# Kernel optimization log

Measured on AMD Instinct MI355X. Metric: run time of the kernel, lower is better.

The kernel has to match this reference:

```python
import jax, jax.numpy as jnp
import numpy as np

NEG_INF = -jnp.inf


def setup_inputs() -> dict:
    key = jax.random.key(0)
    ks = jax.random.split(key, 20)
    B, N, M = 8, 1024, 128
    F_OP, F_MA, F_E, OUT, HID = 64, 64, 16, 64, 128
    inp = {
        "x": jax.random.normal(ks[0], (B, N, F_OP), dtype=jnp.float32),
        "y": jax.random.normal(ks[1], (B, M, F_MA), dtype=jnp.float32),
        "z": jax.random.normal(ks[2], (B, N, M, F_E), dtype=jnp.float32),
        "op_adj_in": jax.random.randint(ks[3], (B, N, N), 0, 2, dtype=jnp.int32),
        "ma_adj_in": jax.random.randint(ks[4], (B, N, N), 0, 2, dtype=jnp.int32),
        "op_ma_adj": jax.random.randint(ks[5], (B, N, M), 0, 2, dtype=jnp.int32),
        # learned parameters
        "weight_op": jax.random.normal(ks[6], (F_OP, OUT), dtype=jnp.float32) * 0.1,
        "weight_ma": jax.random.normal(ks[7], (F_MA, OUT), dtype=jnp.float32) * 0.1,
        "weight_edge": jax.random.normal(ks[8], (F_E, OUT), dtype=jnp.float32) * 0.1,
        "attention_op": jax.random.normal(ks[9], (1, 2 * OUT), dtype=jnp.float32) * 0.1,
        "attention_ma": jax.random.normal(ks[10], (1, 3 * OUT), dtype=jnp.float32) * 0.1,
        "w1": jax.random.normal(ks[11], (2 * OUT, HID), dtype=jnp.float32) * 0.1,
        "b1": jnp.zeros((HID,), dtype=jnp.float32),
        "w2": jax.random.normal(ks[12], (HID, HID), dtype=jnp.float32) * 0.1,
        "b2": jnp.zeros((HID,), dtype=jnp.float32),
        "wo": jax.random.normal(ks[13], (HID, OUT), dtype=jnp.float32) * 0.1,
        "bo": jnp.zeros((OUT,), dtype=jnp.float32),
    }
    return inp


def reference(x, y, z, op_adj_in, ma_adj_in, op_ma_adj,
              weight_op, weight_ma, weight_edge, attention_op, attention_ma,
              w1, b1, w2, b2, wo, bo):
    OUT = weight_op.shape[1]
    h = jnp.einsum('bni,io->bno', x, weight_op)  # [B,N,OUT]
    # all_combinations[b,i,j] = cat(h[b,j], h[b,i]); dot with attention_op splits:
    a1 = attention_op[0, :OUT]
    a2 = attention_op[0, OUT:]
    e_op = (h @ a2)[:, :, None] + (h @ a1)[:, None, :]  # [B,N,N]
    e_op = jax.nn.leaky_relu(e_op, negative_slope=0.01)

    adj = (jnp.swapaxes(op_adj_in, 1, 2) + op_adj_in
           + jnp.swapaxes(ma_adj_in, 1, 2) + ma_adj_in)  # [B,N,N]
    row_mask = jnp.all(op_ma_adj == 0, axis=-1)  # [B,N] ops with no machine link
    adj = jnp.where(row_mask[:, :, None], 1, adj)
    att = jnp.where(adj > 0, e_op, NEG_INF)
    attention_in_op = jax.nn.softmax(att, axis=2)
    h_prime_op = jnp.einsum('bij,bjo->bio', attention_in_op, h)  # [B,N,OUT]

    h_ma = jnp.einsum('bmi,io->bmo', y, weight_ma)  # [B,M,OUT]
    h_edge = jnp.einsum('bnmi,io->bnmo', z, weight_edge)  # [B,N,M,OUT]
    # cat([h_op_i, h_ma_j, h_edge_ij]) @ attention_ma split into three dots
    am1 = attention_ma[0, :OUT]
    am2 = attention_ma[0, OUT:2 * OUT]
    am3 = attention_ma[0, 2 * OUT:]
    e_ma = (h @ am1)[:, :, None] + (h_ma @ am2)[:, None, :] + h_edge @ am3  # [B,N,M]
    e_ma = jax.nn.leaky_relu(e_ma, negative_slope=0.01)

    adj2 = jnp.where(row_mask[:, :, None], 1, op_ma_adj)
    att2 = jnp.where(adj2 > 0, e_ma, NEG_INF)
    attention_in_ma = jax.nn.softmax(att2, axis=2)  # [B,N,M]
    h_ma_edge = h_ma[:, None, :, :] + h_edge  # [B,N,M,OUT]
    h_prime_ma = jnp.einsum('bnm,bnmo->bno', attention_in_ma, h_ma_edge) + h

    h_prime = jnp.concatenate([h_prime_op, h_prime_ma], axis=-1)  # [B,N,2*OUT]
    embed = jax.nn.elu(h_prime @ w1 + b1)
    embed = jax.nn.elu(embed @ w2 + b2)
    embed = embed @ wo + bo
    embed = jnp.where(row_mask[:, :, None], 0.0, embed)
    return embed
```

## Files before the change

### kernel.cpp

```cpp
#include <hip/hip_runtime.h>
#include <math.h>

#define BB 8
#define NN 1024
#define MM 128
#define FOUT 64
#define HIDN 128

#define OFF_H       0
#define OFF_HMA     524288
#define OFF_HA1     589824
#define OFF_HA2     598016
#define OFF_HAM1    606208
#define OFF_HMAAM2  614400
#define OFF_RMASK   615424
#define OFF_WAM3    623616
#define OFF_HPRIME  623632
#define OFF_RDIR    1672208
#define OFF_OPMB    1934352
#define OFF_WT1HI   1967120
#define OFF_WT1LO   1975312
#define OFF_WT2HI   1983504
#define OFF_WT2LO   1991696
#define OFF_WTOHI   1999888
#define OFF_WTOLO   2003984
#define OFF_HTHI    2008080
#define OFF_HTLO    2270224
#define OFF_HMATHI  2532368
#define OFF_HMATLO  2565136
#define OFF_TRM     2597904

typedef __attribute__((ext_vector_type(8))) short bf16x8;
typedef __attribute__((ext_vector_type(8))) unsigned short u16x8;
typedef __attribute__((ext_vector_type(4))) float f32x4;

__device__ __forceinline__ void splitbf(float v, unsigned short& h, unsigned short& l) {
    unsigned u = __float_as_uint(v);
    unsigned hb = (u + 0x7FFFu + ((u >> 16) & 1u)) >> 16;
    float hf = __uint_as_float(hb << 16);
    float lf = v - hf;
    unsigned ul = __float_as_uint(lf);
    unsigned lb = (ul + 0x7FFFu + ((ul >> 16) & 1u)) >> 16;
    h = (unsigned short)hb; l = (unsigned short)lb;
}

__device__ __forceinline__ unsigned short tobf(float v) {
    unsigned u = __float_as_uint(v);
    return (unsigned short)((u + 0x7FFFu + ((u >> 16) & 1u)) >> 16);
}

__global__ __launch_bounds__(256) void k1_prep(
    const float* __restrict__ x, const float* __restrict__ y,
    const int* __restrict__ op_ma_adj,
    const int* __restrict__ op_adj, const int* __restrict__ ma_adj,
    const float* __restrict__ w_op, const float* __restrict__ w_ma,
    const float* __restrict__ w_edge,
    const float* __restrict__ att_op, const float* __restrict__ att_ma,
    const float* __restrict__ w1_g, const float* __restrict__ w2_g,
    const float* __restrict__ wo_g,
    float* __restrict__ h, float* __restrict__ h_ma,
    float* __restrict__ ha1, float* __restrict__ ha2, float* __restrict__ ham1,
    float* __restrict__ hmaam2, int* __restrict__ rmask, float* __restrict__ wam3,
    unsigned long long* __restrict__ rowdir, unsigned long long* __restrict__ opmb,
    unsigned short* __restrict__ trm,
    unsigned short* __restrict__ wt1hi, unsigned short* __restrict__ wt1lo,
    unsigned short* __restrict__ wt2hi, unsigned short* __restrict__ wt2lo,
    unsigned short* __restrict__ wtohi, unsigned short* __restrict__ wtolo,
    unsigned short* __restrict__ hthi, unsigned short* __restrict__ htlo,
    unsigned short* __restrict__ hmathi, unsigned short* __restrict__ hmatlo)
{
    __shared__ float wlds[64 * 64];
    __shared__ unsigned hstage[32 * 64];
    int bid = blockIdx.x;
    int t = threadIdx.x;
    int lane = t & 63;
    int wv = t >> 6;

    if (bid < 256) {
        int b = bid >> 5;
        int n0g = (bid & 31) * 32;
        for (int k = t; k < 4096; k += 256) wlds[k] = w_op[k];
        float a1c = att_op[lane], a2c = att_op[64 + lane], am1c = att_ma[lane];
        __syncthreads();
        #pragma unroll
        for (int p = 0; p < 8; ++p) {
            int row = b * NN + n0g + p * 4 + wv;
            float xv = x[(size_t)row * 64 + lane];
            float acc = 0.f;
            #pragma unroll
            for (int i = 0; i < 64; ++i) {
                float xi = __shfl(xv, i);
                acc += xi * wlds[i * 64 + lane];
            }
            h[(size_t)row * 64 + lane] = acc;
            unsigned short hs, ls;
            splitbf(acc, hs, ls);
            hstage[(p * 4 + wv) * 64 + lane] = (unsigned)hs | ((unsigned)ls << 16);
            float d1 = acc * a1c, d2 = acc * a2c, d3 = acc * am1c;
            #pragma unroll
            for (int m = 32; m; m >>= 1) {
                d1 += __shfl_xor(d1, m);
                d2 += __shfl_xor(d2, m);
                d3 += __shfl_xor(d3, m);
            }
            int v0 = op_ma_adj[(size_t)row * 128 + lane];
            int v1 = op_ma_adj[(size_t)row * 128 + 64 + lane];
            unsigned long long w0 = __ballot(v0 != 0);
            unsigned long long w1 = __ballot(v1 != 0);
            if (lane == 0) {
                ha1[row] = d1; ha2[row] = d2; ham1[row] = d3;
                opmb[row * 2] = w0; opmb[row * 2 + 1] = w1;
                rmask[row] = ((w0 | w1) == 0ULL) ? 1 : 0;
            }
        }
        __syncthreads();
        {
            int plane = t >> 7;
            int q = t & 127;
            int o = q >> 1;
            int hf = q & 1;
            int sh = plane * 16;
            unsigned short* dst = plane ? htlo : hthi;
            u16x8 pk0, pk1;
            #pragma unroll
            for (int k = 0; k < 8; ++k)
                pk0[k] = (unsigned short)((hstage[(hf * 16 + k) * 64 + o] >> sh) & 0xFFFFu);
            #pragma unroll
            for (int k = 0; k < 8; ++k)
                pk1[k] = (unsigned short)((hstage[(hf * 16 + 8 + k) * 64 + o] >> sh) & 0xFFFFu);
            size_t base = ((size_t)((bid >> 5) * 64 + o)) * 1024 + n0g + hf * 16;
            *(u16x8*)&dst[base] = pk0;
            *(u16x8*)&dst[base + 8] = pk1;
        }
    } else if (bid < 288) {
        int bb = (bid - 256) >> 2;
        int m0 = ((bid - 256) & 3) * 32;
        for (int k = t; k < 4096; k += 256) wlds[k] = w_ma[k];
        float am2c = att_ma[64 + lane];
        __syncthreads();
        #pragma unroll
        for (int p = 0; p < 8; ++p) {
            int row = bb * MM + m0 + p * 4 + wv;
            float yv = y[(size_t)row * 64 + lane];
            float acc = 0.f;
            #pragma unroll
            for (int i = 0; i < 64; ++i) {
                float yi = __shfl(yv, i);
                acc += yi * wlds[i * 64 + lane];
            }
            h_ma[(size_t)row * 64 + lane] = acc;
            unsigned short hs, ls;
            splitbf(acc, hs, ls);
            hstage[(p * 4 + wv) * 64 + lane] = (unsigned)hs | ((unsigned)ls << 16);
            float d = acc * am2c;
            #pragma unroll
            for (int m = 32; m; m >>= 1) d += __shfl_xor(d, m);
            if (lane == 0) hmaam2[row] = d;
        }
        __syncthreads();
        {
            int plane = t >> 7;
            int q = t & 127;
            int o = q >> 1;
            int hf = q & 1;
            int sh = plane * 16;
            unsigned short* dst = plane ? hmatlo : hmathi;
            u16x8 pk0, pk1;
            #pragma unroll
            for (int k = 0; k < 8; ++k)
                pk0[k] = (unsigned short)((hstage[(hf * 16 + k) * 64 + o] >> sh) & 0xFFFFu);
            #pragma unroll
            for (int k = 0; k < 8; ++k)
                pk1[k] = (unsigned short)((hstage[(hf * 16 + 8 + k) * 64 + o] >> sh) & 0xFFFFu);
            size_t base = ((size_t)(bb * 64 + o)) * 128 + m0 + hf * 16;
            *(u16x8*)&dst[base] = pk0;
            *(u16x8*)&dst[base + 8] = pk1;
        }
    } else if (bid == 288) {
        if (t < 16) {
            float s = 0.f;
            for (int o = 0; o < 64; ++o) s += w_edge[t * 64 + o] * att_ma[128 + o];
            wam3[t] = s;
        }
    } else if (bid < 2337) {
        unsigned char (*nib)[4][64] = (unsigned char(*)[4][64])wlds;
        int p = bid - 289;
        int b = p >> 8;
        int rg = p & 255;
        int rl = t >> 6;
        int row = rg * 4 + rl;
        const int4* oprow = (const int4*)(op_adj + ((size_t)(b * NN + row)) * NN);
        const int4* marow = (const int4*)(ma_adj + ((size_t)(b * NN + row)) * NN);
        #pragma unroll
        for (int p2 = 0; p2 < 4; ++p2) {
            int4 vo = oprow[p2 * 64 + lane];
            int4 vm = marow[p2 * 64 + lane];
            unsigned nb = ((vo.x | vm.x) ? 1u : 0u) | ((vo.y | vm.y) ? 2u : 0u)
                        | ((vo.z | vm.z) ? 4u : 0u) | ((vo.w | vm.w) ? 8u : 0u);
            nib[rl][p2][lane] = (unsigned char)nb;
        }
        __syncthreads();
        if (t < 64) {
            int arl = t >> 4, q = t & 15;
            const unsigned* nw = (const unsigned*)&nib[arl][q >> 2][(q & 3) * 16];
            unsigned long long w = 0;
            #pragma unroll
            for (int u = 0; u < 4; ++u) {
                unsigned v = nw[u];
                w |= (unsigned long long)(v & 0xFu)         << (16 * u);
                w |= (unsigned long long)((v >> 8) & 0xFu)  << (16 * u + 4);
                w |= (unsigned long long)((v >> 16) & 0xFu) << (16 * u + 8);
                w |= (unsigned long long)((v >> 24) & 0xFu) << (16 * u + 12);
            }
            int jrow = rg * 4 + arl;
            rowdir[((size_t)(b * NN + jrow)) * 16 + q] = w;
            #pragma unroll
            for (int s = 0; s < 4; ++s) {
                trm[((size_t)(b * 64 + q * 4 + s)) * 1024 + jrow] =
                    (unsigned short)((w >> (16 * s)) & 0xFFFFu);
            }
        }
    } else {
        float (*tls)[33] = (float(*)[33])wlds;
        int p = bid - 2337;
        const float* src; unsigned short *dhi, *dlo; int KD, CD, tI, tJ;
        if (p < 16)      { src = w1_g; dhi = wt1hi; dlo = wt1lo; KD = 128; CD = 128; tI = p >> 2; tJ = p & 3; }
        else if (p < 32) { src = w2_g; dhi = wt2hi; dlo = wt2lo; KD = 128; CD = 128; tI = (p-16) >> 2; tJ = (p-16) & 3; }
        else             { src = wo_g; dhi = wtohi; dlo = wtolo; KD = 128; CD = 64;  tI = (p-32) >> 1; tJ = (p-32) & 1; }
        int k0 = tI * 32, c0 = tJ * 32;
        #pragma unroll
        for (int it = 0; it < 4; ++it) {
            int r = (t >> 5) + it * 8;
            int c = t & 31;
            tls[r][c] = src[(size_t)(k0 + r) * CD + c0 + c];
        }
        __syncthreads();
        #pragma unroll
        for (int it = 0; it < 4; ++it) {
            int c = (t >> 5) + it * 8;
            int k = t & 31;
            unsigned short hs, ls;
            splitbf(tls[k][c], hs, ls);
            dhi[(size_t)(c0 + c) * KD + k0 + k] = hs;
            dlo[(size_t)(c0 + c) * KD + k0 + k] = ls;
        }
    }
}

__global__ __launch_bounds__(256) void k2_opatt(
    const unsigned long long* __restrict__ rowdir,
    const unsigned short* __restrict__ trm,
    const unsigned short* __restrict__ hthi,
    const unsigned short* __restrict__ htlo,
    const float* __restrict__ ha1, const float* __restrict__ ha2,
    const int* __restrict__ rmask, float* __restrict__ h_prime)
{
    __shared__ __align__(16) unsigned short Pl[16 * 1024];
    __shared__ float ha1s[1024];
    __shared__ unsigned long long dirw[16][16];
    __shared__ unsigned short trw[1024];
    __shared__ float rdeninv[16];
    int bid = blockIdx.x;
    int b = bid >> 6;
    int i0 = (bid & 63) << 4;
    int t = threadIdx.x;

    {
        int row = t >> 4, w = t & 15;
        dirw[row][w] = rowdir[((size_t)(b * NN + i0 + row)) * 16 + w];
    }
    {
        const unsigned* src = (const unsigned*)(trm + ((size_t)(b * 64 + (i0 >> 4))) * 1024);
        ((unsigned*)trw)[t] = src[t];
        ((unsigned*)trw)[t + 256] = src[t + 256];
    }
    ha1s[t] = ha1[b * NN + t];
    ha1s[t + 256] = ha1[b * NN + t + 256];
    ha1s[t + 512] = ha1[b * NN + t + 512];
    ha1s[t + 768] = ha1[b * NN + t + 768];
    __syncthreads();

    {
        int row = t >> 4, q = t & 15;
        int bn = b * NN + i0 + row;
        float ha2i = ha2[bn];
        unsigned rmf = rmask[bn] ? 1u : 0u;

        float mx = -INFINITY;
        #pragma unroll 8
        for (int jj = 0; jj < 64; ++jj) {
            int j = q + (jj << 4);
            float ev = ha2i + ha1s[j];
            ev = ev > 0.f ? ev : 0.01f * ev;
            unsigned bit = ((unsigned)(dirw[row][jj >> 2] >> (q + ((jj & 3) << 4))) & 1u)
                         | ((unsigned)(trw[j] >> row) & 1u) | rmf;
            if (bit) mx = fmaxf(mx, ev);
        }
        #pragma unroll
        for (int m = 1; m < 16; m <<= 1) mx = fmaxf(mx, __shfl_xor(mx, m));

        float s = 0.f;
        #pragma unroll 4
        for (int jj = 0; jj < 64; ++jj) {
            int j = q + (jj << 4);
            float ev = ha2i + ha1s[j];
            ev = ev > 0.f ? ev : 0.01f * ev;
            unsigned bit = ((unsigned)(dirw[row][jj >> 2] >> (q + ((jj & 3) << 4))) & 1u)
                         | ((unsigned)(trw[j] >> row) & 1u) | rmf;
            float u = bit ? __expf(ev - mx) : 0.f;
            s += u;
            unsigned short pb = tobf(u);
            unsigned byteoff = ((unsigned)(row * 2048 + j * 2)) ^ ((unsigned)((row & 7) << 4));
            *(unsigned short*)((char*)Pl + byteoff) = pb;
        }
        #pragma unroll
        for (int m = 1; m < 16; m <<= 1) s += __shfl_xor(s, m);
        if (q == 0) rdeninv[row] = 1.f / s;
    }
    __syncthreads();

    {
        int lane = t & 63, wvv = t >> 6;
        int arow = lane & 15, kg = lane >> 4;
        int col = wvv * 16 + arow;
        const unsigned short* bhp = hthi + ((size_t)(b * 64 + col)) * 1024;
        f32x4 acc = {0.f, 0.f, 0.f, 0.f};
        #pragma unroll 8
        for (int kst = 0; kst < 32; ++kst) {
            unsigned cc = ((unsigned)(kst * 4 + kg)) ^ ((unsigned)(arow & 7));
            bf16x8 pa = *(const bf16x8*)((char*)Pl + arow * 2048 + cc * 16);
            bf16x8 vh = *(const bf16x8*)&bhp[kst * 32 + kg * 8];
            acc = __builtin_amdgcn_mfma_f32_16x16x32_bf16(pa, vh, acc, 0, 0, 0);
        }
        size_t base = (size_t)(b * NN + i0);
        #pragma unroll
        for (int r = 0; r < 4; ++r) {
            int orow = kg * 4 + r;
            float v = acc[r] * rdeninv[orow];
            h_prime[(base + orow) * 128 + col] = v;
        }
    }
}

__global__ __launch_bounds__(256) void k3_maatt(
    const float* __restrict__ z, const unsigned long long* __restrict__ opmb,
    const float* __restrict__ h,
    const unsigned short* __restrict__ hmathi, const unsigned short* __restrict__ hmatlo,
    const float* __restrict__ ham1, const float* __restrict__ hmaam2,
    const int* __restrict__ rmask, const float* __restrict__ wam3,
    const float* __restrict__ w_edge, float* __restrict__ h_prime)
{
    __shared__ __align__(16) unsigned short U_lds[16 * 136];
    __shared__ float wedge_s[1024];
    __shared__ float wam3s[16];
    __shared__ float zsum_s[16][16];
    __shared__ float rdeninv[16];

    int bid = blockIdx.x;
    int b = bid >> 6;
    int n0 = (bid & 63) * 16;
    int t = threadIdx.x;
    int lane = t & 63;
    int wv = t >> 6;

    for (int k = t; k < 1024; k += 256) wedge_s[k] = w_edge[k];
    if (t < 16) wam3s[t] = wam3[t];
    __syncthreads();

    float hm0 = hmaam2[b * MM + lane];
    float hm1 = hmaam2[b * MM + 64 + lane];

    for (int pp = 0; pp < 4; ++pp) {
        int nl = pp * 4 + wv;
        int bn = b * NN + n0 + nl;
        const float4* zr = (const float4*)(z + (size_t)bn * MM * 16);
        float4 a0 = zr[lane * 4 + 0];
        float4 a1 = zr[lane * 4 + 1];
        float4 a2 = zr[lane * 4 + 2];
        float4 a3 = zr[lane * 4 + 3];
        float4 c0 = zr[(lane + 64) * 4 + 0];
        float4 c1 = zr[(lane + 64) * 4 + 1];
        float4 c2 = zr[(lane + 64) * 4 + 2];
        float4 c3 = zr[(lane + 64) * 4 + 3];

        float base = ham1[bn];
        float e0 = base + hm0;
        float e1 = base + hm1;
        e0 += a0.x*wam3s[0] + a0.y*wam3s[1] + a0.z*wam3s[2] + a0.w*wam3s[3]
            + a1.x*wam3s[4] + a1.y*wam3s[5] + a1.z*wam3s[6] + a1.w*wam3s[7]
            + a2.x*wam3s[8] + a2.y*wam3s[9] + a2.z*wam3s[10] + a2.w*wam3s[11]
            + a3.x*wam3s[12] + a3.y*wam3s[13] + a3.z*wam3s[14] + a3.w*wam3s[15];
        e1 += c0.x*wam3s[0] + c0.y*wam3s[1] + c0.z*wam3s[2] + c0.w*wam3s[3]
            + c1.x*wam3s[4] + c1.y*wam3s[5] + c1.z*wam3s[6] + c1.w*wam3s[7]
            + c2.x*wam3s[8] + c2.y*wam3s[9] + c2.z*wam3s[10] + c2.w*wam3s[11]
            + c3.x*wam3s[12] + c3.y*wam3s[13] + c3.z*wam3s[14] + c3.w*wam3s[15];
        e0 = e0 > 0.f ? e0 : 0.01f * e0;
        e1 = e1 > 0.f ? e1 : 0.01f * e1;
        unsigned long long bits0 = opmb[(size_t)bn * 2];
        unsigned long long bits1 = opmb[(size_t)bn * 2 + 1];
        int rm = rmask[bn];
        int v0 = rm | (int)((bits0 >> lane) & 1ULL);
        int v1 = rm | (int)((bits1 >> lane) & 1ULL);
        e0 = v0 ? e0 : -INFINITY;
        e1 = v1 ? e1 : -INFINITY;

        float mx = fmaxf(e0, e1);
        #pragma unroll
        for (int msk = 32; msk; msk >>= 1) mx = fmaxf(mx, __shfl_xor(mx, msk));
        float u0 = __expf(e0 - mx);
        float u1 = __expf(e1 - mx);
        float s = u0 + u1;
        #pragma unroll
        for (int msk = 32; msk; msk >>= 1) s += __shfl_xor(s, msk);

        U_lds[nl * 136 + lane] = tobf(u0);
        U_lds[nl * 136 + 64 + lane] = tobf(u1);
        if (lane == 0) rdeninv[nl] = 1.f / s;

        float zv[16];
        zv[0]=u0*a0.x+u1*c0.x;  zv[1]=u0*a0.y+u1*c0.y;
        zv[2]=u0*a0.z+u1*c0.z;  zv[3]=u0*a0.w+u1*c0.w;
        zv[4]=u0*a1.x+u1*c1.x;  zv[5]=u0*a1.y+u1*c1.y;
        zv[6]=u0*a1.z+u1*c1.z;  zv[7]=u0*a1.w+u1*c1.w;
        zv[8]=u0*a2.x+u1*c2.x;  zv[9]=u0*a2.y+u1*c2.y;
        zv[10]=u0*a2.z+u1*c2.z; zv[11]=u0*a2.w+u1*c2.w;
        zv[12]=u0*a3.x+u1*c3.x; zv[13]=u0*a3.y+u1*c3.y;
        zv[14]=u0*a3.z+u1*c3.z; zv[15]=u0*a3.w+u1*c3.w;
        #pragma unroll
        for (int s2 = 0; s2 < 8; ++s2) {
            float sel = (lane & 1) ? zv[s2] : zv[s2 + 8];
            float got = __shfl_xor(sel, 1);
            zv[s2] = ((lane & 1) ? zv[s2 + 8] : zv[s2]) + got;
        }
        #pragma unroll
        for (int s2 = 0; s2 < 4; ++s2) {
            float sel = (lane & 2) ? zv[s2] : zv[s2 + 4];
            float got = __shfl_xor(sel, 2);
            zv[s2] = ((lane & 2) ? zv[s2 + 4] : zv[s2]) + got;
        }
        #pragma unroll
        for (int s2 = 0; s2 < 2; ++s2) {
            float sel = (lane & 4) ? zv[s2] : zv[s2 + 2];
            float got = __shfl_xor(sel, 4);
            zv[s2] = ((lane & 4) ? zv[s2 + 2] : zv[s2]) + got;
        }
        {
            float sel = (lane & 8) ? zv[0] : zv[1];
            float got = __shfl_xor(sel, 8);
            zv[0] = ((lane & 8) ? zv[1] : zv[0]) + got;
        }
        zv[0] += __shfl_xor(zv[0], 16);
        zv[0] += __shfl_xor(zv[0], 32);
        if (lane < 16) {
            int comp = ((lane & 1) << 3) | ((lane & 2) << 1) | ((lane & 4) >> 1) | ((lane & 8) >> 3);
            zsum_s[nl][comp] = zv[0];
        }
    }
    __syncthreads();

    {
        int arow = lane & 15, kg = lane >> 4;
        int col = wv * 16 + arow;
        bf16x8 ua[4];
        #pragma unroll
        for (int ks = 0; ks < 4; ++ks)
            ua[ks] = *(const bf16x8*)&U_lds[arow * 136 + kg * 8 + ks * 32];
        const unsigned short* bhp = hmathi + ((size_t)(b * 64 + col)) * 128 + kg * 8;
        f32x4 acc = {0.f, 0.f, 0.f, 0.f};
        #pragma unroll
        for (int ks = 0; ks < 4; ++ks) {
            bf16x8 bh = *(const bf16x8*)&bhp[ks * 32];
            acc = __builtin_amdgcn_mfma_f32_16x16x32_bf16(ua[ks], bh, acc, 0, 0, 0);
        }
        #pragma unroll
        for (int r = 0; r < 4; ++r) {
            int row = kg * 4 + r;
            float he = 0.f;
            #pragma unroll
            for (int i = 0; i < 16; ++i) he += zsum_s[row][i] * wedge_s[i * 64 + col];
            int bn = b * NN + n0 + row;
            float val = (acc[r] + he) * rdeninv[row] + h[(size_t)bn * 64 + col];
            h_prime[(size_t)bn * 128 + 64 + col] = val;
        }
    }
}

__global__ __launch_bounds__(256) void k4_mlp(
    const float* __restrict__ hp, const int* __restrict__ rmask,
    const unsigned short* __restrict__ wt1hi, const unsigned short* __restrict__ wt1lo,
    const unsigned short* __restrict__ wt2hi, const unsigned short* __restrict__ wt2lo,
    const unsigned short* __restrict__ wtohi, const unsigned short* __restrict__ wtolo,
    const float* __restrict__ b1, const float* __restrict__ b2,
    const float* __restrict__ bo, float* __restrict__ out)
{
    __shared__ __align__(16) unsigned short Ahi0[16 * 136];
    __shared__ __align__(16) unsigned short Alo0[16 * 136];
    __shared__ __align__(16) unsigned short Ahi1[16 * 136];
    __shared__ __align__(16) unsigned short Alo1[16 * 136];
    __shared__ __align__(16) unsigned short Whi[64 * 128];
    __shared__ __align__(16) unsigned short Wlo[64 * 128];
    __shared__ int rml[16];
    int t = threadIdx.x;
    int lane = t & 63;
    int wv = t >> 6;
    int row0 = blockIdx.x * 16;
    int plane = t >> 7;
    int q = t & 127;

    {
        int r = t >> 4;
        int cg = (t & 15) * 8;
        const float* src = hp + (size_t)(row0 + r) * 128 + cg;
        float4 v0 = *(const float4*)src;
        float4 v1 = *(const float4*)(src + 4);
        float xs[8] = {v0.x, v0.y, v0.z, v0.w, v1.x, v1.y, v1.z, v1.w};
        u16x8 hv, lv;
        #pragma unroll
        for (int j = 0; j < 8; ++j) {
            unsigned short hs, ls;
            splitbf(xs[j], hs, ls);
            hv[j] = hs; lv[j] = ls;
        }
        *(u16x8*)&Ahi0[r * 136 + cg] = hv;
        *(u16x8*)&Alo0[r * 136 + cg] = lv;
        if (t < 16) rml[t] = rmask[row0 + t];
    }
    __syncthreads();

    int arow = lane & 15;
    int kg = lane >> 4;
    int aoff = arow * 136 + kg * 8;
    int lcol = wv * 16 + arow;

    {
        bf16x8 ah[4], al[4];
        #pragma unroll
        for (int ks = 0; ks < 4; ++ks) {
            ah[ks] = *(const bf16x8*)&Ahi0[aoff + ks * 32];
            al[ks] = *(const bf16x8*)&Alo0[aoff + ks * 32];
        }
        #pragma unroll
        for (int half = 0; half < 2; ++half) {
            __syncthreads();
            {
                const unsigned short* gsrc = plane ? wt1lo : wt1hi;
                char* dst = (char*)(plane ? Wlo : Whi);
                #pragma unroll
                for (int i = 0; i < 8; ++i) {
                    int L = q * 8 + i;
                    int col = L >> 4, kc = L & 15;
                    u16x8 v = *(const u16x8*)&gsrc[(size_t)(half * 64 + col) * 128 + kc * 8];
                    unsigned byteoff = ((unsigned)(col * 256 + kc * 16)) ^ ((unsigned)((col & 7) << 4));
                    *(u16x8*)(dst + byteoff) = v;
                }
            }
            __syncthreads();
            int col = half * 64 + lcol;
            f32x4 acc = {0.f, 0.f, 0.f, 0.f};
            #pragma unroll
            for (int ks = 0; ks < 4; ++ks) {
                unsigned wb = ((unsigned)(lcol * 256 + kg * 16 + ks * 64)) ^ ((unsigned)((arow & 7) << 4));
                bf16x8 bh = *(const bf16x8*)((char*)Whi + wb);
                bf16x8 bl = *(const bf16x8*)((char*)Wlo + wb);
                acc = __builtin_amdgcn_mfma_f32_16x16x32_bf16(ah[ks], bh, acc, 0, 0, 0);
                acc = __builtin_amdgcn_mfma_f32_16x16x32_bf16(al[ks], bh, acc, 0, 0, 0);
                acc = __builtin_amdgcn_mfma_f32_16x16x32_bf16(ah[ks], bl, acc, 0, 0, 0);
            }
            float bb = b1[col];
            #pragma unroll
            for (int r = 0; r < 4; ++r) {
                int row = kg * 4 + r;
                float v = acc[r] + bb;
                v = v > 0.f ? v : __expf(v) - 1.f;
                unsigned short hs, ls;
                splitbf(v, hs, ls);
                Ahi1[row * 136 + col] = hs;
                Alo1[row * 136 + col] = ls;
            }
        }
    }
    __syncthreads();

    {
        bf16x8 ah[4], al[4];
        #pragma unroll
        for (int ks = 0; ks < 4; ++ks) {
            ah[ks] = *(const bf16x8*)&Ahi1[aoff + ks * 32];
            al[ks] = *(const bf16x8*)&Alo1[aoff + ks * 32];
        }
        #pragma unroll
        for (int half = 0; half < 2; ++half) {
            __syncthreads();
            {
                const unsigned short* gsrc = plane ? wt2lo : wt2hi;
                char* dst = (char*)(plane ? Wlo : Whi);
                #pragma unroll
                for (int i = 0; i < 8; ++i) {
                    int L = q * 8 + i;
                    int col = L >> 4, kc = L & 15;
                    u16x8 v = *(const u16x8*)&gsrc[(size_t)(half * 64 + col) * 128 + kc * 8];
                    unsigned byteoff = ((unsigned)(col * 256 + kc * 16)) ^ ((unsigned)((col & 7) << 4));
                    *(u16x8*)(dst + byteoff) = v;
                }
            }
            __syncthreads();
            int col = half * 64 + lcol;
            f32x4 acc = {0.f, 0.f, 0.f, 0.f};
            #pragma unroll
            for (int ks = 0; ks < 4; ++ks) {
                unsigned wb = ((unsigned)(lcol * 256 + kg * 16 + ks * 64)) ^ ((unsigned)((arow & 7) << 4));
                bf16x8 bh = *(const bf16x8*)((char*)Whi + wb);
                bf16x8 bl = *(const bf16x8*)((char*)Wlo + wb);
                acc = __builtin_amdgcn_mfma_f32_16x16x32_bf16(ah[ks], bh, acc, 0, 0, 0);
                acc = __builtin_amdgcn_mfma_f32_16x16x32_bf16(al[ks], bh, acc, 0, 0, 0);
                acc = __builtin_amdgcn_mfma_f32_16x16x32_bf16(ah[ks], bl, acc, 0, 0, 0);
            }
            float bb = b2[col];
            #pragma unroll
            for (int r = 0; r < 4; ++r) {
                int row = kg * 4 + r;
                float v = acc[r] + bb;
                v = v > 0.f ? v : __expf(v) - 1.f;
                unsigned short hs, ls;
                splitbf(v, hs, ls);
                Ahi0[row * 136 + col] = hs;
                Alo0[row * 136 + col] = ls;
            }
        }
    }
    __syncthreads();

    {
        bf16x8 ah[4], al[4];
        #pragma unroll
        for (int ks = 0; ks < 4; ++ks) {
            ah[ks] = *(const bf16x8*)&Ahi0[aoff + ks * 32];
            al[ks] = *(const bf16x8*)&Alo0[aoff + ks * 32];
        }
        __syncthreads();
        {
            const unsigned short* gsrc = plane ? wtolo : wtohi;
            char* dst = (char*)(plane ? Wlo : Whi);
            #pragma unroll
            for (int i = 0; i < 8; ++i) {
                int L = q * 8 + i;
                int col = L >> 4, kc = L & 15;
                u16x8 v = *(const u16x8*)&gsrc[(size_t)col * 128 + kc * 8];
                unsigned byteoff = ((unsigned)(col * 256 + kc * 16)) ^ ((unsigned)((col & 7) << 4));
                *(u16x8*)(dst + byteoff) = v;
            }
        }
        __syncthreads();
        int col = lcol;
        f32x4 acc = {0.f, 0.f, 0.f, 0.f};
        #pragma unroll
        for (int ks = 0; ks < 4; ++ks) {
            unsigned wb = ((unsigned)(lcol * 256 + kg * 16 + ks * 64)) ^ ((unsigned)((arow & 7) << 4));
            bf16x8 bh = *(const bf16x8*)((char*)Whi + wb);
            bf16x8 bl = *(const bf16x8*)((char*)Wlo + wb);
            acc = __builtin_amdgcn_mfma_f32_16x16x32_bf16(ah[ks], bh, acc, 0, 0, 0);
            acc = __builtin_amdgcn_mfma_f32_16x16x32_bf16(al[ks], bh, acc, 0, 0, 0);
            acc = __builtin_amdgcn_mfma_f32_16x16x32_bf16(ah[ks], bl, acc, 0, 0, 0);
        }
        float bb = bo[col];
        #pragma unroll
        for (int r = 0; r < 4; ++r) {
            int row = kg * 4 + r;
            float v = acc[r] + bb;
            out[(size_t)(row0 + row) * 64 + col] = rml[row] ? 0.f : v;
        }
    }
}

extern "C" void kernel_launch(void* const* d_in, const int* in_sizes, int n_in,
                              void* d_out, int out_size, void* d_ws, size_t ws_size,
                              hipStream_t stream) {
    const float* x      = (const float*)d_in[0];
    const float* y      = (const float*)d_in[1];
    const float* z      = (const float*)d_in[2];
    const int*   op_adj = (const int*)d_in[3];
    const int*   ma_adj = (const int*)d_in[4];
    const int*   opma   = (const int*)d_in[5];
    const float* w_op   = (const float*)d_in[6];
    const float* w_ma   = (const float*)d_in[7];
    const float* w_edge = (const float*)d_in[8];
    const float* att_op = (const float*)d_in[9];
    const float* att_ma = (const float*)d_in[10];
    const float* w1     = (const float*)d_in[11];
    const float* b1     = (const float*)d_in[12];
    const float* w2     = (const float*)d_in[13];
    const float* b2     = (const float*)d_in[14];
    const float* wo     = (const float*)d_in[15];
    const float* bo     = (const float*)d_in[16];
    float* out = (float*)d_out;

    float* ws = (float*)d_ws;
    float* h       = ws + OFF_H;
    float* h_ma    = ws + OFF_HMA;
    float* ha1     = ws + OFF_HA1;
    float* ha2     = ws + OFF_HA2;
    float* ham1    = ws + OFF_HAM1;
    float* hmaam2  = ws + OFF_HMAAM2;
    int*   rmask   = (int*)(ws + OFF_RMASK);
    float* wam3    = ws + OFF_WAM3;
    float* h_prime = ws + OFF_HPRIME;
    unsigned long long* rowdir = (unsigned long long*)(ws + OFF_RDIR);
    unsigned long long* opmb = (unsigned long long*)(ws + OFF_OPMB);
    unsigned short* trm   = (unsigned short*)(ws + OFF_TRM);
    unsigned short* wt1hi = (unsigned short*)(ws + OFF_WT1HI);
    unsigned short* wt1lo = (unsigned short*)(ws + OFF_WT1LO);
    unsigned short* wt2hi = (unsigned short*)(ws + OFF_WT2HI);
    unsigned short* wt2lo = (unsigned short*)(ws + OFF_WT2LO);
    unsigned short* wtohi = (unsigned short*)(ws + OFF_WTOHI);
    unsigned short* wtolo = (unsigned short*)(ws + OFF_WTOLO);
    unsigned short* hthi  = (unsigned short*)(ws + OFF_HTHI);
    unsigned short* htlo  = (unsigned short*)(ws + OFF_HTLO);
    unsigned short* hmathi = (unsigned short*)(ws + OFF_HMATHI);
    unsigned short* hmatlo = (unsigned short*)(ws + OFF_HMATLO);

    k1_prep<<<256 + 32 + 1 + 2048 + 40, 256, 0, stream>>>(
        x, y, opma, op_adj, ma_adj, w_op, w_ma, w_edge, att_op, att_ma,
        w1, w2, wo,
        h, h_ma, ha1, ha2, ham1, hmaam2, rmask, wam3, rowdir, opmb, trm,
        wt1hi, wt1lo, wt2hi, wt2lo, wtohi, wtolo, hthi, htlo, hmathi, hmatlo);

    k2_opatt<<<512, 256, 0, stream>>>(
        rowdir, trm, hthi, htlo, ha1, ha2, rmask, h_prime);

    k3_maatt<<<512, 256, 0, stream>>>(
        z, opmb, h, hmathi, hmatlo, ham1, hmaam2, rmask, wam3, w_edge, h_prime);

    k4_mlp<<<512, 256, 0, stream>>>(
        h_prime, rmask, wt1hi, wt1lo, wt2hi, wt2lo, wtohi, wtolo,
        b1, b2, bo, out);
}
```

Before: 84.21 us.

## Move adjacency packing into machine-attention kernel and simplify op-attention max pass

```diff
diff --git a/kernel.cpp b/kernel.cpp
--- a/kernel.cpp
+++ b/kernel.cpp
@@ -49,10 +49,9 @@
     return (unsigned short)((u + 0x7FFFu + ((u >> 16) & 1u)) >> 16);
 }
 
-__global__ __launch_bounds__(256) void k1_prep(
+__global__ __launch_bounds__(256) void kA_prep(
     const float* __restrict__ x, const float* __restrict__ y,
     const int* __restrict__ op_ma_adj,
-    const int* __restrict__ op_adj, const int* __restrict__ ma_adj,
     const float* __restrict__ w_op, const float* __restrict__ w_ma,
     const float* __restrict__ w_edge,
     const float* __restrict__ att_op, const float* __restrict__ att_ma,
@@ -61,8 +60,7 @@
     float* __restrict__ h, float* __restrict__ h_ma,
     float* __restrict__ ha1, float* __restrict__ ha2, float* __restrict__ ham1,
     float* __restrict__ hmaam2, int* __restrict__ rmask, float* __restrict__ wam3,
-    unsigned long long* __restrict__ rowdir, unsigned long long* __restrict__ opmb,
-    unsigned short* __restrict__ trm,
+    unsigned long long* __restrict__ opmb,
     unsigned short* __restrict__ wt1hi, unsigned short* __restrict__ wt1lo,
     unsigned short* __restrict__ wt2hi, unsigned short* __restrict__ wt2lo,
     unsigned short* __restrict__ wtohi, unsigned short* __restrict__ wtolo,
@@ -128,7 +126,7 @@
             #pragma unroll
             for (int k = 0; k < 8; ++k)
                 pk1[k] = (unsigned short)((hstage[(hf * 16 + 8 + k) * 64 + o] >> sh) & 0xFFFFu);
-            size_t base = ((size_t)((bid >> 5) * 64 + o)) * 1024 + n0g + hf * 16;
+            size_t base = ((size_t)(b * 64 + o)) * 1024 + n0g + hf * 16;
             *(u16x8*)&dst[base] = pk0;
             *(u16x8*)&dst[base + 8] = pk1;
         }
@@ -182,47 +180,9 @@
             for (int o = 0; o < 64; ++o) s += w_edge[t * 64 + o] * att_ma[128 + o];
             wam3[t] = s;
         }
-    } else if (bid < 2337) {
-        unsigned char (*nib)[4][64] = (unsigned char(*)[4][64])wlds;
-        int p = bid - 289;
-        int b = p >> 8;
-        int rg = p & 255;
-        int rl = t >> 6;
-        int row = rg * 4 + rl;
-        const int4* oprow = (const int4*)(op_adj + ((size_t)(b * NN + row)) * NN);
-        const int4* marow = (const int4*)(ma_adj + ((size_t)(b * NN + row)) * NN);
-        #pragma unroll
-        for (int p2 = 0; p2 < 4; ++p2) {
-            int4 vo = oprow[p2 * 64 + lane];
-            int4 vm = marow[p2 * 64 + lane];
-            unsigned nb = ((vo.x | vm.x) ? 1u : 0u) | ((vo.y | vm.y) ? 2u : 0u)
-                        | ((vo.z | vm.z) ? 4u : 0u) | ((vo.w | vm.w) ? 8u : 0u);
-            nib[rl][p2][lane] = (unsigned char)nb;
-        }
-        __syncthreads();
-        if (t < 64) {
-            int arl = t >> 4, q = t & 15;
-            const unsigned* nw = (const unsigned*)&nib[arl][q >> 2][(q & 3) * 16];
-            unsigned long long w = 0;
-            #pragma unroll
-            for (int u = 0; u < 4; ++u) {
-                unsigned v = nw[u];
-                w |= (unsigned long long)(v & 0xFu)         << (16 * u);
-                w |= (unsigned long long)((v >> 8) & 0xFu)  << (16 * u + 4);
-                w |= (unsigned long long)((v >> 16) & 0xFu) << (16 * u + 8);
-                w |= (unsigned long long)((v >> 24) & 0xFu) << (16 * u + 12);
-            }
-            int jrow = rg * 4 + arl;
-            rowdir[((size_t)(b * NN + jrow)) * 16 + q] = w;
-            #pragma unroll
-            for (int s = 0; s < 4; ++s) {
-                trm[((size_t)(b * 64 + q * 4 + s)) * 1024 + jrow] =
-                    (unsigned short)((w >> (16 * s)) & 0xFFFFu);
-            }
-        }
     } else {
         float (*tls)[33] = (float(*)[33])wlds;
-        int p = bid - 2337;
+        int p = bid - 289;
         const float* src; unsigned short *dhi, *dlo; int KD, CD, tI, tJ;
         if (p < 16)      { src = w1_g; dhi = wt1hi; dlo = wt1lo; KD = 128; CD = 128; tI = p >> 2; tJ = p & 3; }
         else if (p < 32) { src = w2_g; dhi = wt2hi; dlo = wt2lo; KD = 128; CD = 128; tI = (p-16) >> 2; tJ = (p-16) & 3; }
@@ -247,121 +207,69 @@
     }
 }
 
-__global__ __launch_bounds__(256) void k2_opatt(
-    const unsigned long long* __restrict__ rowdir,
-    const unsigned short* __restrict__ trm,
-    const unsigned short* __restrict__ hthi,
-    const unsigned short* __restrict__ htlo,
-    const float* __restrict__ ha1, const float* __restrict__ ha2,
-    const int* __restrict__ rmask, float* __restrict__ h_prime)
-{
-    __shared__ __align__(16) unsigned short Pl[16 * 1024];
-    __shared__ float ha1s[1024];
-    __shared__ unsigned long long dirw[16][16];
-    __shared__ unsigned short trw[1024];
-    __shared__ float rdeninv[16];
-    int bid = blockIdx.x;
-    int b = bid >> 6;
-    int i0 = (bid & 63) << 4;
-    int t = threadIdx.x;
-
-    {
-        int row = t >> 4, w = t & 15;
-        dirw[row][w] = rowdir[((size_t)(b * NN + i0 + row)) * 16 + w];
-    }
-    {
-        const unsigned* src = (const unsigned*)(trm + ((size_t)(b * 64 + (i0 >> 4))) * 1024);
-        ((unsigned*)trw)[t] = src[t];
-        ((unsigned*)trw)[t + 256] = src[t + 256];
-    }
-    ha1s[t] = ha1[b * NN + t];
-    ha1s[t + 256] = ha1[b * NN + t + 256];
-    ha1s[t + 512] = ha1[b * NN + t + 512];
-    ha1s[t + 768] = ha1[b * NN + t + 768];
-    __syncthreads();
-
-    {
-        int row = t >> 4, q = t & 15;
-        int bn = b * NN + i0 + row;
-        float ha2i = ha2[bn];
-        unsigned rmf = rmask[bn] ? 1u : 0u;
-
-        float mx = -INFINITY;
-        #pragma unroll 8
-        for (int jj = 0; jj < 64; ++jj) {
-            int j = q + (jj << 4);
-            float ev = ha2i + ha1s[j];
-            ev = ev > 0.f ? ev : 0.01f * ev;
-            unsigned bit = ((unsigned)(dirw[row][jj >> 2] >> (q + ((jj & 3) << 4))) & 1u)
-                         | ((unsigned)(trw[j] >> row) & 1u) | rmf;
-            if (bit) mx = fmaxf(mx, ev);
-        }
-        #pragma unroll
-        for (int m = 1; m < 16; m <<= 1) mx = fmaxf(mx, __shfl_xor(mx, m));
-
-        float s = 0.f;
-        #pragma unroll 4
-        for (int jj = 0; jj < 64; ++jj) {
-            int j = q + (jj << 4);
-            float ev = ha2i + ha1s[j];
-            ev = ev > 0.f ? ev : 0.01f * ev;
-            unsigned bit = ((unsigned)(dirw[row][jj >> 2] >> (q + ((jj & 3) << 4))) & 1u)
-                         | ((unsigned)(trw[j] >> row) & 1u) | rmf;
-            float u = bit ? __expf(ev - mx) : 0.f;
-            s += u;
-            unsigned short pb = tobf(u);
-            unsigned byteoff = ((unsigned)(row * 2048 + j * 2)) ^ ((unsigned)((row & 7) << 4));
-            *(unsigned short*)((char*)Pl + byteoff) = pb;
-        }
-        #pragma unroll
-        for (int m = 1; m < 16; m <<= 1) s += __shfl_xor(s, m);
-        if (q == 0) rdeninv[row] = 1.f / s;
-    }
-    __syncthreads();
-
-    {
-        int lane = t & 63, wvv = t >> 6;
-        int arow = lane & 15, kg = lane >> 4;
-        int col = wvv * 16 + arow;
-        const unsigned short* bhp = hthi + ((size_t)(b * 64 + col)) * 1024;
-        f32x4 acc = {0.f, 0.f, 0.f, 0.f};
-        #pragma unroll 8
-        for (int kst = 0; kst < 32; ++kst) {
-            unsigned cc = ((unsigned)(kst * 4 + kg)) ^ ((unsigned)(arow & 7));
-            bf16x8 pa = *(const bf16x8*)((char*)Pl + arow * 2048 + cc * 16);
-            bf16x8 vh = *(const bf16x8*)&bhp[kst * 32 + kg * 8];
-            acc = __builtin_amdgcn_mfma_f32_16x16x32_bf16(pa, vh, acc, 0, 0, 0);
-        }
-        size_t base = (size_t)(b * NN + i0);
-        #pragma unroll
-        for (int r = 0; r < 4; ++r) {
-            int orow = kg * 4 + r;
-            float v = acc[r] * rdeninv[orow];
-            h_prime[(base + orow) * 128 + col] = v;
-        }
-    }
-}
-
-__global__ __launch_bounds__(256) void k3_maatt(
+__global__ __launch_bounds__(256) void kB_pack_ma(
+    const int* __restrict__ op_adj, const int* __restrict__ ma_adj,
+    unsigned long long* __restrict__ rowdir, unsigned short* __restrict__ trm,
     const float* __restrict__ z, const unsigned long long* __restrict__ opmb,
-    const float* __restrict__ h,
-    const unsigned short* __restrict__ hmathi, const unsigned short* __restrict__ hmatlo,
+    const float* __restrict__ h, const unsigned short* __restrict__ hmathi,
     const float* __restrict__ ham1, const float* __restrict__ hmaam2,
     const int* __restrict__ rmask, const float* __restrict__ wam3,
     const float* __restrict__ w_edge, float* __restrict__ h_prime)
 {
+    __shared__ unsigned char nib[4][4][64];
     __shared__ __align__(16) unsigned short U_lds[16 * 136];
     __shared__ float wedge_s[1024];
     __shared__ float wam3s[16];
     __shared__ float zsum_s[16][16];
     __shared__ float rdeninv[16];
 
-    int bid = blockIdx.x;
-    int b = bid >> 6;
-    int n0 = (bid & 63) * 16;
     int t = threadIdx.x;
     int lane = t & 63;
     int wv = t >> 6;
+
+    if (blockIdx.x < 2048) {
+        int p = blockIdx.x;
+        int b = p >> 8;
+        int rg = p & 255;
+        int rl = t >> 6;
+        int row = rg * 4 + rl;
+        const int4* oprow = (const int4*)(op_adj + ((size_t)(b * NN + row)) * NN);
+        const int4* marow = (const int4*)(ma_adj + ((size_t)(b * NN + row)) * NN);
+        #pragma unroll
+        for (int p2 = 0; p2 < 4; ++p2) {
+            int4 vo = oprow[p2 * 64 + lane];
+            int4 vm = marow[p2 * 64 + lane];
+            unsigned nb = ((vo.x | vm.x) ? 1u : 0u) | ((vo.y | vm.y) ? 2u : 0u)
+                        | ((vo.z | vm.z) ? 4u : 0u) | ((vo.w | vm.w) ? 8u : 0u);
+            nib[rl][p2][lane] = (unsigned char)nb;
+        }
+        __syncthreads();
+        if (t < 64) {
+            int arl = t >> 4, q = t & 15;
+            const unsigned* nw = (const unsigned*)&nib[arl][q >> 2][(q & 3) * 16];
+            unsigned long long w = 0;
+            #pragma unroll
+            for (int u = 0; u < 4; ++u) {
+                unsigned v = nw[u];
+                w |= (unsigned long long)(v & 0xFu)         << (16 * u);
+                w |= (unsigned long long)((v >> 8) & 0xFu)  << (16 * u + 4);
+                w |= (unsigned long long)((v >> 16) & 0xFu) << (16 * u + 8);
+                w |= (unsigned long long)((v >> 24) & 0xFu) << (16 * u + 12);
+            }
+            int jrow = rg * 4 + arl;
+            rowdir[((size_t)(b * NN + jrow)) * 16 + q] = w;
+            #pragma unroll
+            for (int s = 0; s < 4; ++s) {
+                trm[((size_t)(b * 64 + q * 4 + s)) * 1024 + jrow] =
+                    (unsigned short)((w >> (16 * s)) & 0xFFFFu);
+            }
+        }
+        return;
+    }
+
+    int bid = blockIdx.x - 2048;
+    int b = bid >> 6;
+    int n0 = (bid & 63) * 16;
 
     for (int k = t; k < 1024; k += 256) wedge_s[k] = w_edge[k];
     if (t < 16) wam3s[t] = wam3[t];
@@ -485,7 +393,101 @@
     }
 }
 
-__global__ __launch_bounds__(256) void k4_mlp(
+__global__ __launch_bounds__(256) void kC_opatt(
+    const unsigned long long* __restrict__ rowdir,
+    const unsigned short* __restrict__ trm,
+    const unsigned short* __restrict__ hthi,
+    const float* __restrict__ ha1, const float* __restrict__ ha2,
+    const int* __restrict__ rmask, float* __restrict__ h_prime)
+{
+    __shared__ __align__(16) unsigned short Pl[16 * 1024];
+    __shared__ float ha1s[1024];
+    __shared__ unsigned long long dirw[16][16];
+    __shared__ unsigned short trw[1024];
+    __shared__ float rdeninv[16];
+    int bid = blockIdx.x;
+    int b = bid >> 6;
+    int i0 = (bid & 63) << 4;
+    int t = threadIdx.x;
+
+    {
+        int row = t >> 4, w = t & 15;
+        dirw[row][w] = rowdir[((size_t)(b * NN + i0 + row)) * 16 + w];
+    }
+    {
+        const unsigned* src = (const unsigned*)(trm + ((size_t)(b * 64 + (i0 >> 4))) * 1024);
+        ((unsigned*)trw)[t] = src[t];
+        ((unsigned*)trw)[t + 256] = src[t + 256];
+    }
+    ha1s[t] = ha1[b * NN + t];
+    ha1s[t + 256] = ha1[b * NN + t + 256];
+    ha1s[t + 512] = ha1[b * NN + t + 512];
+    ha1s[t + 768] = ha1[b * NN + t + 768];
+    __syncthreads();
+
+    {
+        int row = t >> 4, q = t & 15;
+        int bn = b * NN + i0 + row;
+        float ha2i = ha2[bn];
+        unsigned rmf = rmask[bn] ? 1u : 0u;
+
+        float mh = -INFINITY;
+        #pragma unroll 8
+        for (int jj = 0; jj < 64; ++jj) {
+            int j = q + (jj << 4);
+            unsigned bit = ((unsigned)(dirw[row][jj >> 2] >> (q + ((jj & 3) << 4))) & 1u)
+                         | ((unsigned)(trw[j] >> row) & 1u) | rmf;
+            if (bit) mh = fmaxf(mh, ha1s[j]);
+        }
+        #pragma unroll
+        for (int m = 1; m < 16; m <<= 1) mh = fmaxf(mh, __shfl_xor(mh, m));
+        float mx = ha2i + mh;
+        mx = mx > 0.f ? mx : 0.01f * mx;
+
+        float s = 0.f;
+        #pragma unroll 4
+        for (int jj = 0; jj < 64; ++jj) {
+            int j = q + (jj << 4);
+            float ev = ha2i + ha1s[j];
+            ev = ev > 0.f ? ev : 0.01f * ev;
+            unsigned bit = ((unsigned)(dirw[row][jj >> 2] >> (q + ((jj & 3) << 4))) & 1u)
+                         | ((unsigned)(trw[j] >> row) & 1u) | rmf;
+            float u = bit ? __expf(ev - mx) : 0.f;
+            s += u;
+            unsigned short pb = tobf(u);
+            unsigned byteoff = ((unsigned)(row * 2048 + j * 2)) ^ ((unsigned)((row & 7) << 4));
+            *(unsigned short*)((char*)Pl + byteoff) = pb;
+        }
+        #pragma unroll
+        for (int m = 1; m < 16; m <<= 1) s += __shfl_xor(s, m);
+        if (q == 0) rdeninv[row] = 1.f / s;
+    }
+    __syncthreads();
+
+    {
+        int lane = t & 63, wvv = t >> 6;
+        int arow = lane & 15, kg = lane >> 4;
+        int col = wvv * 16 + arow;
+        const unsigned short* bhp = hthi + ((size_t)(b * 64 + col)) * 1024;
+        f32x4 acc = {0.f, 0.f, 0.f, 0.f};
+        #pragma unroll 8
+        for (int kst = 0; kst < 32; ++kst) {
+            unsigned cc = ((unsigned)(kst * 4 + kg)) ^ ((unsigned)(arow & 7));
+            bf16x8 pa = *(const bf16x8*)((char*)Pl + arow * 2048 + cc * 16);
+            bf16x8 vh = *(const bf16x8*)&bhp[kst * 32 + kg * 8];
+            acc = __builtin_amdgcn_mfma_f32_16x16x32_bf16(pa, vh, acc, 0, 0, 0);
+        }
+        size_t base = (size_t)(b * NN + i0);
+        #pragma unroll
+        for (int r = 0; r < 4; ++r) {
+            int orow = kg * 4 + r;
+            float v = acc[r] * rdeninv[orow];
+            h_prime[(base + orow) * 128 + col] = v;
+        }
+    }
+}
+
+__global__ __launch_bounds__(256) void kD_mlp(
     const float* __restrict__ hp, const int* __restrict__ rmask,
     const unsigned short* __restrict__ wt1hi, const unsigned short* __restrict__ wt1lo,
     const unsigned short* __restrict__ wt2hi, const unsigned short* __restrict__ wt2lo,
@@ -718,19 +720,19 @@
     unsigned short* hmathi = (unsigned short*)(ws + OFF_HMATHI);
     unsigned short* hmatlo = (unsigned short*)(ws + OFF_HMATLO);
 
-    k1_prep<<<256 + 32 + 1 + 2048 + 40, 256, 0, stream>>>(
-        x, y, opma, op_adj, ma_adj, w_op, w_ma, w_edge, att_op, att_ma,
-        w1, w2, wo,
-        h, h_ma, ha1, ha2, ham1, hmaam2, rmask, wam3, rowdir, opmb, trm,
+    kA_prep<<<329, 256, 0, stream>>>(
+        x, y, opma, w_op, w_ma, w_edge, att_op, att_ma, w1, w2, wo,
+        h, h_ma, ha1, ha2, ham1, hmaam2, rmask, wam3, opmb,
         wt1hi, wt1lo, wt2hi, wt2lo, wtohi, wtolo, hthi, htlo, hmathi, hmatlo);
 
-    k2_opatt<<<512, 256, 0, stream>>>(
-        rowdir, trm, hthi, htlo, ha1, ha2, rmask, h_prime);
-
-    k3_maatt<<<512, 256, 0, stream>>>(
-        z, opmb, h, hmathi, hmatlo, ham1, hmaam2, rmask, wam3, w_edge, h_prime);
-
-    k4_mlp<<<512, 256, 0, stream>>>(
+    kB_pack_ma<<<2560, 256, 0, stream>>>(
+        op_adj, ma_adj, rowdir, trm,
+        z, opmb, h, hmathi, ham1, hmaam2, rmask, wam3, w_edge, h_prime);
+
+    kC_opatt<<<512, 256, 0, stream>>>(
+        rowdir, trm, hthi, ha1, ha2, rmask, h_prime);
+
+    kD_mlp<<<512, 256, 0, stream>>>(
         h_prime, rmask, wt1hi, wt1lo, wt2hi, wt2lo, wtohi, wtolo,
         b1, b2, bo, out);
 }
```

Result: slower. 93.02 us (+10.5%).
